# Optimization experiments

Measured on AMD Instinct MI355X. Metric: run time of the kernel, lower is better.

Reference implementation:

```python
import jax, jax.numpy as jnp
import numpy as np

N = 200000   # nodes
E = 800000   # edges
G = 10000    # graphs in batch
H = 128      # hidden_channels
IN_NODE = 26  # 10-2 + 16 + 2
IN_EDGE = 13  # 4-3 + 8 + 2*2


def setup_inputs() -> dict:
    key = jax.random.key(0)
    ks = jax.random.split(key, 30)
    f = lambda i, shape: (jax.random.normal(ks[i], shape, jnp.float32) * 0.1)
    inp = {}
    inp['atom_num'] = jax.random.randint(ks[0], (N,), 0, 119)
    inp['atom_arom'] = jax.random.randint(ks[1], (N,), 0, 2)
    inp['x_cont'] = f(2, (N, 8))
    inp['bond_type'] = jax.random.randint(ks[3], (E,), 0, 22)
    inp['edge_cont'] = f(4, (E, 1))
    inp['bond_conj'] = jax.random.randint(ks[5], (E,), 0, 2)
    inp['bond_arom'] = jax.random.randint(ks[6], (E,), 0, 2)
    inp['edge_index'] = jax.random.randint(ks[7], (2, E), 0, N)
    inp['batch'] = jnp.sort(jax.random.randint(ks[8], (N,), 0, G))
    # embeddings (padding rows zeroed, matching padding_idx)
    inp['atom_emb'] = f(9, (119, 16)).at[0].set(0.0)
    inp['bond_emb'] = f(10, (22, 8)).at[0].set(0.0)
    inp['bool_emb'] = f(11, (3, 2)).at[2].set(0.0)
    # GATv2 layer 1 (gnn1)
    inp['Wl1'] = f(12, (IN_NODE, H)); inp['bl1'] = f(13, (H,))
    inp['Wr1'] = f(14, (IN_NODE, H)); inp['br1'] = f(15, (H,))
    inp['We1'] = f(16, (IN_EDGE, H))
    inp['att1'] = f(17, (H,)); inp['bias1'] = f(18, (H,))
    # GATv2 shared layer (gnn) -- used for layers 2 and 3 with the SAME weights
    inp['Wl2'] = f(19, (H, H)); inp['bl2'] = f(20, (H,))
    inp['Wr2'] = f(21, (H, H)); inp['br2'] = f(22, (H,))
    inp['We2'] = f(23, (IN_EDGE, H))
    inp['att2'] = f(24, (H,)); inp['bias2'] = f(25, (H,))
    return inp


def _gatv2(x, src, dst, ea, Wl, bl, Wr, br, We, att, bias):
    """PyG GATv2Conv, heads=1, add_self_loops=True, fill_value='mean'."""
    n = x.shape[0]
    # self-loop edge features = mean of incoming edge features per node
    deg = jax.ops.segment_sum(jnp.ones((src.shape[0],), x.dtype), dst, num_segments=n)
    ea_mean = jax.ops.segment_sum(ea, dst, num_segments=n) / jnp.clip(deg, 1.0)[:, None]
    loop = jnp.arange(n, dtype=src.dtype)
    s = jnp.concatenate([src, loop])
    d = jnp.concatenate([dst, loop])
    ea_full = jnp.concatenate([ea, ea_mean], axis=0)
    xl = x @ Wl + bl   # source transform
    xr = x @ Wr + br   # destination transform
    m = xl[s] + xr[d] + ea_full @ We           # [E+N, H]
    m = jax.nn.leaky_relu(m, 0.2)
    logits = m @ att                            # [E+N]
    mx = jax.ops.segment_max(logits, d, num_segments=n)
    a = jnp.exp(logits - mx[d])
    denom = jax.ops.segment_sum(a, d, num_segments=n)
    alpha = a / denom[d]
    out = jax.ops.segment_sum(alpha[:, None] * xl[s], d, num_segments=n)
    return out + bias


def reference(atom_num, atom_arom, x_cont, bond_type, edge_cont, bond_conj,
              bond_arom, edge_index, batch, atom_emb, bond_emb, bool_emb,
              Wl1, bl1, Wr1, br1, We1, att1, bias1,
              Wl2, bl2, Wr2, br2, We2, att2, bias2):
    src, dst = edge_index[0], edge_index[1]
    x = jnp.concatenate([atom_emb[atom_num], x_cont, bool_emb[atom_arom]], axis=1)  # [N,26]
    ea = jnp.concatenate([bond_emb[bond_type], edge_cont,
                          bool_emb[bond_conj], bool_emb[bond_arom]], axis=1)        # [E,13]
    h = jax.nn.relu(_gatv2(x, src, dst, ea, Wl1, bl1, Wr1, br1, We1, att1, bias1))
    # num_layers_gnn=3 -> shared-weight layer applied twice (dropout off in eval)
    h = jax.nn.relu(_gatv2(h, src, dst, ea, Wl2, bl2, Wr2, br2, We2, att2, bias2))
    h = jax.nn.relu(_gatv2(h, src, dst, ea, Wl2, bl2, Wr2, br2, We2, att2, bias2))
    pooled = jax.ops.segment_max(h, batch, num_segments=G)  # global_max_pool
    pooled = jnp.where(jnp.isfinite(pooled), pooled, 0.0)   # guard empty graphs
    return pooled
```

## Files before the change

kernel.cpp:

```cpp
#include <hip/hip_runtime.h>
#include <hip/hip_bf16.h>
#include <cstdint>
#include <cstdio>


typedef __attribute__((ext_vector_type(8))) short bf16x8;
typedef __attribute__((ext_vector_type(8))) unsigned short u16x8;
typedef __attribute__((ext_vector_type(4))) float f32x4;

#define TBT_S 132

static __device__ __forceinline__ float leaky02(float v) { return v > 0.f ? v : 0.2f * v; }
static __device__ __forceinline__ float b2f(unsigned short u) {
    return __uint_as_float(((unsigned)u) << 16);
}
static __device__ __forceinline__ unsigned short f2b(float f) {
    __hip_bfloat16 h = __float2bfloat16(f);
    return *(unsigned short*)&h;
}


__global__ __launch_bounds__(256) void prep_init(
    int* __restrict__ degcnt, int n_degcnt,
    int* __restrict__ outz, int n_out,
    const float* __restrict__ Wl2, const float* __restrict__ Wr2,
    __hip_bfloat16* __restrict__ Wp,
    const float* __restrict__ Wl1, const float* __restrict__ Wr1,
    __hip_bfloat16* __restrict__ Wp1,
    const int* __restrict__ atom_num, const int* __restrict__ atom_arom,
    const float* __restrict__ x_cont, const float* __restrict__ atom_emb,
    const float* __restrict__ bool_emb, __hip_bfloat16* __restrict__ Xf, int N,
    int e_z1, int e_z2, int e_pw, int e_pw1)
{
    int b = blockIdx.x;
    if (b < e_z1) {
        int i = b * 256 + threadIdx.x;
        if (i < n_degcnt) degcnt[i] = 0;
    } else if (b < e_z2) {
        int i = (b - e_z1) * 256 + threadIdx.x;
        if (i < n_out) outz[i] = 0;
    } else if (b < e_pw) {
        int idx = (b - e_z2) * 256 + threadIdx.x;
        int j    = idx & 7;
        int lane = (idx >> 3) & 63;
        int ks   = (idx >> 9) & 3;
        int nt   = idx >> 11;
        int k = ks * 32 + ((lane >> 4) << 3) + j;
        int n = nt * 16 + (lane & 15);
        float v = (n < 128) ? Wl2[k * 128 + n] : Wr2[k * 128 + (n - 128)];
        Wp[idx] = __float2bfloat16(v);
    } else if (b < e_pw1) {
        int idx = (b - e_pw) * 256 + threadIdx.x;
        int j    = idx & 7;
        int lane = (idx >> 3) & 63;
        int ntc  = idx >> 9;
        int k = ((lane >> 4) << 3) + j;
        int n = ntc * 16 + (lane & 15);
        float v = 0.f;
        if (k < 26) v = (n < 128) ? Wl1[k * 128 + n] : Wr1[k * 128 + (n - 128)];
        Wp1[idx] = __float2bfloat16(v);
    } else {
        int n = (b - e_pw1) * 256 + threadIdx.x;
        if (n >= N) return;
        int an = atom_num[n], am = atom_arom[n];
        unsigned short v[32];
#pragma unroll
        for (int k = 0; k < 16; k++) v[k] = f2b(atom_emb[an * 16 + k]);
#pragma unroll
        for (int k = 0; k < 8; k++)  v[16 + k] = f2b(x_cont[(size_t)n * 8 + k]);
        v[24] = f2b(bool_emb[am * 2]);
        v[25] = f2b(bool_emb[am * 2 + 1]);
#pragma unroll
        for (int k = 26; k < 32; k++) v[k] = 0;
        unsigned short* dst = (unsigned short*)Xf + (size_t)n * 32;
#pragma unroll
        for (int q = 0; q < 4; q++)
            *(u16x8*)(dst + q * 8) = *(const u16x8*)&v[q * 8];
    }
}


__global__ __launch_bounds__(256) void count_deg(
    const int* __restrict__ dst, int* __restrict__ deg, int E)
{
    int e = blockIdx.x * 256 + threadIdx.x;
    if (e < E) atomicAdd(&deg[dst[e]], 1);
}

#define SORT_BLK 1024

__global__ __launch_bounds__(256) void sort_hist(
    const int* __restrict__ deg, int* __restrict__ block_hist, int N)
{
    __shared__ int h[512];
    for (int i = threadIdx.x; i < 512; i += 256) h[i] = 0;
    __syncthreads();
    int base = blockIdx.x * SORT_BLK;
#pragma unroll
    for (int k = 0; k < 4; k++) {
        int n = base + k * 256 + threadIdx.x;
        if (n < N) {
            int d = deg[n]; if (d > 511) d = 511;
            atomicAdd(&h[d], 1);
        }
    }
    __syncthreads();
    for (int i = threadIdx.x; i < 512; i += 256)
        block_hist[blockIdx.x * 512 + i] = h[i];
}

__global__ __launch_bounds__(512) void sort_scan(
    int* __restrict__ block_hist, int* __restrict__ bin_base,
    int* __restrict__ edge_base, int nsb)
{
    __shared__ int s[512];
    int t = threadIdx.x;
    int acc = 0;
    for (int b = 0; b < nsb; b++) {
        int v = block_hist[b * 512 + t];
        block_hist[b * 512 + t] = acc;
        acc += v;
    }
    s[t] = acc;
    __syncthreads();
    for (int off = 1; off < 512; off <<= 1) {
        int x = (t >= off) ? s[t - off] : 0;
        __syncthreads();
        s[t] += x;
        __syncthreads();
    }
    bin_base[t] = s[t] - acc;
    __syncthreads();
    int ec = acc * t;
    s[t] = ec;
    __syncthreads();
    for (int off = 1; off < 512; off <<= 1) {
        int x = (t >= off) ? s[t - off] : 0;
        __syncthreads();
        s[t] += x;
        __syncthreads();
    }
    edge_base[t] = s[t] - ec;
}

__global__ __launch_bounds__(256) void sort_scatter(
    const int* __restrict__ deg, const int* __restrict__ block_hist,
    const int* __restrict__ bin_base, const int* __restrict__ edge_base,
    int4* __restrict__ meta, int* __restrict__ nrp, int N)
{
    __shared__ int h[512];
    for (int i = threadIdx.x; i < 512; i += 256) h[i] = 0;
    __syncthreads();
    int bs = blockIdx.x;
    int base = bs * SORT_BLK;
#pragma unroll
    for (int k = 0; k < 4; k++) {
        int n = base + k * 256 + threadIdx.x;
        if (n < N) {
            int d = deg[n]; if (d > 511) d = 511;
            int r = atomicAdd(&h[d], 1);
            int posInBin = block_hist[bs * 512 + d] + r;
            int pos = bin_base[d] + posInBin;
            int rp = edge_base[d] + posInBin * d;
            int4 m; m.x = rp; m.y = d; m.z = n; m.w = 0;
            meta[pos] = m;
            nrp[n] = rp;
        }
    }
}

__global__ __launch_bounds__(256) void csr_fill(
    const int* __restrict__ src, const int* __restrict__ dst,
    const int* __restrict__ bond_type, const float* __restrict__ edge_cont,
    const int* __restrict__ bond_conj, const int* __restrict__ bond_arom,
    const int* __restrict__ nrp, int* __restrict__ cnt,
    int4* __restrict__ csr_rec, int E)
{
    int e = blockIdx.x * 256 + threadIdx.x;
    if (e >= E) return;
    int d = dst[e];
    int pos = nrp[d] + atomicAdd(&cnt[d], 1);
    int codes = (bond_type[e] & 0xFF) | ((bond_conj[e] & 1) << 8) | ((bond_arom[e] & 1) << 16);
    int4 rec;
    rec.x = src[e];
    rec.y = codes;
    rec.z = __float_as_int(edge_cont[e]);
    rec.w = 0;
    csr_rec[pos] = rec;
}


__global__ __launch_bounds__(256) void gemm_mfma1(
    const __hip_bfloat16* __restrict__ Xf,
    const __hip_bfloat16* __restrict__ Wp,
    const float* __restrict__ bl, const float* __restrict__ br,
    __hip_bfloat16* __restrict__ XL, __hip_bfloat16* __restrict__ XR, int N)
{
    __shared__ unsigned short sT[64 * 256];
    int lane = threadIdx.x & 63;
    int wave = threadIdx.x >> 6;
    int row0 = blockIdx.x * 64;
    int m_lane = lane & 15;
    int quad = lane >> 4;
    const unsigned short* Xu = (const unsigned short*)Xf;
    const unsigned short* Wu = (const unsigned short*)Wp;

    f32x4 acc[4][4];
#pragma unroll
    for (int mt = 0; mt < 4; mt++)
#pragma unroll
        for (int nt = 0; nt < 4; nt++) acc[mt][nt] = (f32x4){0.f, 0.f, 0.f, 0.f};

    bf16x8 a[4], b[4];
#pragma unroll
    for (int mt = 0; mt < 4; mt++)
        a[mt] = *(const bf16x8*)(Xu + (size_t)(row0 + mt * 16 + m_lane) * 32 + quad * 8);
#pragma unroll
    for (int nt = 0; nt < 4; nt++)
        b[nt] = *(const bf16x8*)(Wu + ((wave * 4 + nt) * 64 + lane) * 8);
#pragma unroll
    for (int mt = 0; mt < 4; mt++)
#pragma unroll
        for (int nt = 0; nt < 4; nt++)
            acc[mt][nt] = __builtin_amdgcn_mfma_f32_16x16x32_bf16(
                a[mt], b[nt], acc[mt][nt], 0, 0, 0);

#pragma unroll
    for (int nt = 0; nt < 4; nt++) {
        int col = wave * 64 + nt * 16 + m_lane;
        float bv = (col < 128) ? bl[col] : br[col - 128];
#pragma unroll
        for (int mt = 0; mt < 4; mt++) {
            int rbase = mt * 16 + quad * 4;
#pragma unroll
            for (int reg = 0; reg < 4; reg++)
                sT[(rbase + reg) * 256 + col] = f2b(acc[mt][nt][reg] + bv);
        }
    }

    __syncthreads();

    unsigned short* XLu = (unsigned short*)XL;
    unsigned short* XRu = (unsigned short*)XR;
    int t = threadIdx.x;
#pragma unroll
    for (int q = 0; q < 4; q++) {
        int s = t * 32 + q * 8;
        int r = s >> 7, c = s & 127;
        *(u16x8*)(XLu + (size_t)(row0 + r) * 128 + c) = *(const u16x8*)&sT[r * 256 + c];
        *(u16x8*)(XRu + (size_t)(row0 + r) * 128 + c) = *(const u16x8*)&sT[r * 256 + 128 + c];
    }
}

__global__ __launch_bounds__(256) void gemm_mfma(
    const __hip_bfloat16* H,
    const __hip_bfloat16* __restrict__ Wp,
    const float* __restrict__ bl, const float* __restrict__ br,
    __hip_bfloat16* __restrict__ XL, __hip_bfloat16* XR, int N)
{
    __shared__ unsigned short sT[64 * 256];
    int lane = threadIdx.x & 63;
    int wave = threadIdx.x >> 6;
    int row0 = blockIdx.x * 64;
    int m_lane = lane & 15;
    int quad = lane >> 4;
    const unsigned short* Hu = (const unsigned short*)H;
    const unsigned short* Wu = (const unsigned short*)Wp;

    f32x4 acc[4][4];
#pragma unroll
    for (int mt = 0; mt < 4; mt++)
#pragma unroll
        for (int nt = 0; nt < 4; nt++) acc[mt][nt] = (f32x4){0.f, 0.f, 0.f, 0.f};

#pragma unroll
    for (int ks = 0; ks < 4; ks++) {
        int koff = ks * 32 + quad * 8;
        bf16x8 a[4], b[4];
#pragma unroll
        for (int mt = 0; mt < 4; mt++)
            a[mt] = *(const bf16x8*)(Hu + (size_t)(row0 + mt * 16 + m_lane) * 128 + koff);
#pragma unroll
        for (int nt = 0; nt < 4; nt++)
            b[nt] = *(const bf16x8*)(Wu + ((((wave * 4 + nt) * 4) + ks) * 64 + lane) * 8);
#pragma unroll
        for (int mt = 0; mt < 4; mt++)
#pragma unroll
            for (int nt = 0; nt < 4; nt++)
                acc[mt][nt] = __builtin_amdgcn_mfma_f32_16x16x32_bf16(
                    a[mt], b[nt], acc[mt][nt], 0, 0, 0);
    }

#pragma unroll
    for (int nt = 0; nt < 4; nt++) {
        int col = wave * 64 + nt * 16 + m_lane;
        float bv = (col < 128) ? bl[col] : br[col - 128];
#pragma unroll
        for (int mt = 0; mt < 4; mt++) {
            int rbase = mt * 16 + quad * 4;
#pragma unroll
            for (int reg = 0; reg < 4; reg++)
                sT[(rbase + reg) * 256 + col] = f2b(acc[mt][nt][reg] + bv);
        }
    }

    __syncthreads();

    unsigned short* XLu = (unsigned short*)XL;
    unsigned short* XRu = (unsigned short*)XR;
    int t = threadIdx.x;
#pragma unroll
    for (int q = 0; q < 4; q++) {
        int s = t * 32 + q * 8;
        int r = s >> 7, c = s & 127;
        *(u16x8*)(XLu + (size_t)(row0 + r) * 128 + c) = *(const u16x8*)&sT[r * 256 + c];
        *(u16x8*)(XRu + (size_t)(row0 + r) * 128 + c) = *(const u16x8*)&sT[r * 256 + 128 + c];
    }
}

__global__ __launch_bounds__(256) void gat_fused(
    const int4* __restrict__ meta, const int4* __restrict__ csr_rec,
    const float* __restrict__ bond_emb, const float* __restrict__ bool_emb,
    const __hip_bfloat16* __restrict__ XL, const __hip_bfloat16* XR,
    const float* __restrict__ We,
    const float* __restrict__ att,
    const float* __restrict__ bias,
    __hip_bfloat16* OUT, int N)
{
    __shared__ float sTbt[22 * TBT_S];
    __shared__ float sTca[4 * TBT_S];
    __shared__ float sW8[128];

    for (int i = threadIdx.x; i < 22 * 128; i += 256) {
        int bt = i >> 7, c = i & 127;
        float s = 0.f;
#pragma unroll
        for (int k = 0; k < 8; k++) s = fmaf(bond_emb[bt * 8 + k], We[k * 128 + c], s);
        sTbt[bt * TBT_S + c] = s;
    }
    for (int i = threadIdx.x; i < 4 * 128; i += 256) {
        int idx = i >> 7, c = i & 127;
        int cj = idx >> 1, ar = idx & 1;
        float s = bool_emb[cj * 2]     * We[9 * 128 + c]
                + bool_emb[cj * 2 + 1] * We[10 * 128 + c]
                + bool_emb[ar * 2]     * We[11 * 128 + c]
                + bool_emb[ar * 2 + 1] * We[12 * 128 + c];
        sTca[idx * TBT_S + c] = s;
    }
    if (threadIdx.x < 128) sW8[threadIdx.x] = We[8 * 128 + threadIdx.x];
    __syncthreads();

    int lane = threadIdx.x & 63;
    int wave = threadIdx.x >> 6;
    int sl   = lane & 15;
    int sw   = lane >> 4;
    int cbase = sl * 8;

    float a8[8], bs8[8], w88[8];
    {
        float4 t0 = *(const float4*)&att[cbase],  t1 = *(const float4*)&att[cbase + 4];
        float4 u0 = *(const float4*)&bias[cbase], u1 = *(const float4*)&bias[cbase + 4];
        float4 v0 = *(const float4*)&sW8[cbase],  v1 = *(const float4*)&sW8[cbase + 4];
#pragma unroll
        for (int i = 0; i < 4; i++) {
            a8[i] = (&t0.x)[i];  a8[i + 4] = (&t1.x)[i];
            bs8[i] = (&u0.x)[i]; bs8[i + 4] = (&u1.x)[i];
            w88[i] = (&v0.x)[i]; w88[i + 4] = (&v1.x)[i];
        }
    }

    const unsigned short* XLu = (const unsigned short*)XL;
    const unsigned short* XRu = (const unsigned short*)XR;
    unsigned short* OUTu = (unsigned short*)OUT;

    int group = (blockIdx.x * 4 + wave) * 4 + sw;
    int stride = gridDim.x * 16;

    int4 mt;
    if (group < N) mt = meta[group];

    for (int idx = group; idx < N; idx += stride) {
        int rp = mt.x, dg = mt.y, n = mt.z;
        u16x8 uxr = *(const u16x8*)(XRu + (size_t)n * 128 + cbase);
        u16x8 un  = *(const u16x8*)(XLu + (size_t)n * 128 + cbase);
        int nidx = idx + stride;
        int4 mt_n = meta[(nidx < N) ? nidx : idx];

        float xr[8];
#pragma unroll
        for (int i = 0; i < 8; i++) xr[i] = b2f(uxr[i]);

        float runs = 0.f;
        float acc[8], ets[8];
#pragma unroll
        for (int i = 0; i < 8; i++) { acc[i] = 0.f; ets[i] = 0.f; }

        for (int j = 0; j < dg; j += 4) {
            int cnt = dg - j; if (cnt > 4) cnt = 4;
            int4 rec[4];
#pragma unroll
            for (int jj = 0; jj < 4; jj++)
                if (jj < cnt) rec[jj] = csr_rec[rp + j + jj];
            u16x8 uv[4];
#pragma unroll
            for (int jj = 0; jj < 4; jj++)
                if (jj < cnt)
                    uv[jj] = *(const u16x8*)(XLu + (size_t)rec[jj].x * 128 + cbase);

            float part[4];
#pragma unroll
            for (int jj = 0; jj < 4; jj++) {
                if (jj >= cnt) continue;
                int bt = rec[jj].y & 0xFF;
                int ca = (((rec[jj].y >> 8) & 1) << 1) | ((rec[jj].y >> 16) & 1);
                float ec = __int_as_float(rec[jj].z);
                const float* tb = &sTbt[bt * TBT_S + cbase];
                const float* tc = &sTca[ca * TBT_S + cbase];
                float p = 0.f;
#pragma unroll
                for (int i = 0; i < 8; i++) {
                    float et = fmaf(ec, w88[i], tb[i] + tc[i]);
                    ets[i] += et;
                    float m = leaky02(xr[i] + b2f(uv[jj][i]) + et);
                    p = fmaf(m, a8[i], p);
                }
                p += __shfl_xor(p, 1);
                p += __shfl_xor(p, 2);
                p += __shfl_xor(p, 4);
                p += __shfl_xor(p, 8);
                part[jj] = p;
            }
#pragma unroll
            for (int jj = 0; jj < 4; jj++) {
                if (jj >= cnt) continue;
                float wgt = __expf(part[jj]);
                runs += wgt;
#pragma unroll
                for (int i = 0; i < 8; i++)
                    acc[i] = fmaf(wgt, b2f(uv[jj][i]), acc[i]);
            }
        }

        {
            float invd = 1.f / (float)(dg > 0 ? dg : 1);
            float p = 0.f;
#pragma unroll
            for (int i = 0; i < 8; i++) {
                float m = leaky02(xr[i] + b2f(un[i]) + ets[i] * invd);
                p = fmaf(m, a8[i], p);
            }
            p += __shfl_xor(p, 1);
            p += __shfl_xor(p, 2);
            p += __shfl_xor(p, 4);
            p += __shfl_xor(p, 8);
            float wgt = __expf(p);
            runs += wgt;
#pragma unroll
            for (int i = 0; i < 8; i++)
                acc[i] = fmaf(wgt, b2f(un[i]), acc[i]);
        }

        float inv = 1.f / runs;
        u16x8 o;
#pragma unroll
        for (int i = 0; i < 8; i++)
            o[i] = f2b(fmaxf(fmaf(acc[i], inv, bs8[i]), 0.f));
        *(u16x8*)(OUTu + (size_t)n * 128 + cbase) = o;

        mt = mt_n;
    }
}

__global__ __launch_bounds__(128) void pool_max(
    const __hip_bfloat16* __restrict__ H, const int* __restrict__ batch,
    float* __restrict__ out, int N)
{
    int c = threadIdx.x;
    int n0 = blockIdx.x * 64;
    int nend = n0 + 64; if (nend > N) nend = N;
    const unsigned short* Hu = (const unsigned short*)H;
    int g_cur = -1;
    float acc = 0.f;
    for (int n = n0; n < nend; ++n) {
        int g = batch[n];
        if (g != g_cur) {
            if (g_cur >= 0)
                atomicMax((int*)out + (size_t)g_cur * 128 + c, __float_as_int(acc));
            g_cur = g;
            acc = 0.f;
        }
        acc = fmaxf(acc, b2f(Hu[(size_t)n * 128 + c]));
    }
    if (g_cur >= 0)
        atomicMax((int*)out + (size_t)g_cur * 128 + c, __float_as_int(acc));
}


static inline size_t align_up(size_t x, size_t a) { return (x + a - 1) & ~(a - 1); }
static inline int cdiv(int a, int b) { return (a + b - 1) / b; }

extern "C" void kernel_launch(void* const* d_in, const int* in_sizes, int n_in,
                              void* d_out, int out_size, void* d_ws, size_t ws_size,
                              hipStream_t stream)
{
    const int N = in_sizes[0];
    const int E = in_sizes[3];

    const int*   atom_num  = (const int*)d_in[0];
    const int*   atom_arom = (const int*)d_in[1];
    const float* x_cont    = (const float*)d_in[2];
    const int*   bond_type = (const int*)d_in[3];
    const float* edge_cont = (const float*)d_in[4];
    const int*   bond_conj = (const int*)d_in[5];
    const int*   bond_arom = (const int*)d_in[6];
    const int*   e_src     = (const int*)d_in[7];
    const int*   e_dst     = e_src + E;
    const int*   batch     = (const int*)d_in[8];
    const float* atom_emb  = (const float*)d_in[9];
    const float* bond_emb  = (const float*)d_in[10];
    const float* bool_emb  = (const float*)d_in[11];
    const float* Wl1 = (const float*)d_in[12]; const float* bl1 = (const float*)d_in[13];
    const float* Wr1 = (const float*)d_in[14]; const float* br1 = (const float*)d_in[15];
    const float* We1 = (const float*)d_in[16]; const float* att1 = (const float*)d_in[17];
    const float* bias1 = (const float*)d_in[18];
    const float* Wl2 = (const float*)d_in[19]; const float* bl2 = (const float*)d_in[20];
    const float* Wr2 = (const float*)d_in[21]; const float* br2 = (const float*)d_in[22];
    const float* We2 = (const float*)d_in[23]; const float* att2 = (const float*)d_in[24];
    const float* bias2 = (const float*)d_in[25];
    float* out = (float*)d_out;

    const int nsb = cdiv(N, SORT_BLK);

    char* w = (char*)d_ws;
    size_t off = 0;
    auto alloc = [&](size_t bytes) {
        void* p = w + off;
        off = align_up(off + bytes, 256);
        return p;
    };
    __hip_bfloat16* A  = (__hip_bfloat16*)alloc((size_t)N * 128 * 2);
    __hip_bfloat16* B  = (__hip_bfloat16*)alloc((size_t)N * 128 * 2);
    __hip_bfloat16* Xf = (__hip_bfloat16*)alloc((size_t)N * 32 * 2);
    __hip_bfloat16* Wp = (__hip_bfloat16*)alloc((size_t)32768 * 2);
    __hip_bfloat16* Wp1= (__hip_bfloat16*)alloc((size_t)8192 * 2);
    int*   degcnt  = (int*)alloc((size_t)2 * N * 4);
    int*   deg     = degcnt;
    int*   cnt     = degcnt + N;
    int4*  csr_rec = (int4*)alloc((size_t)E * 16);
    int4*  meta    = (int4*)alloc((size_t)N * 16);
    int*   nrp     = (int*)alloc((size_t)N * 4);
    int*   block_hist = (int*)alloc((size_t)nsb * 512 * 4);
    int*   bin_base   = (int*)alloc(512 * 4);
    int*   edge_base  = (int*)alloc(512 * 4);
    size_t required = off;

    fprintf(stderr, "[GNN] ws_size=%zu required=%zu%s\n", ws_size, required,
            ws_size < required ? "  INSUFFICIENT - skipping" : "");
    if (ws_size < required) return;

    int bz1 = cdiv(2 * N, 256);
    int bz2 = cdiv(out_size, 256);
    int bpw = 32768 / 256;
    int bpw1 = 8192 / 256;
    int bbx = cdiv(N, 256);
    int e_z1 = bz1, e_z2 = e_z1 + bz2, e_pw = e_z2 + bpw, e_pw1 = e_pw + bpw1;
    prep_init<<<e_pw1 + bbx, 256, 0, stream>>>(
        degcnt, 2 * N, (int*)out, out_size,
        Wl2, Wr2, Wp, Wl1, Wr1, Wp1,
        atom_num, atom_arom, x_cont, atom_emb, bool_emb, Xf, N,
        e_z1, e_z2, e_pw, e_pw1);

    count_deg<<<cdiv(E, 256), 256, 0, stream>>>(e_dst, deg, E);
    sort_hist<<<nsb, 256, 0, stream>>>(deg, block_hist, N);
    sort_scan<<<1, 512, 0, stream>>>(block_hist, bin_base, edge_base, nsb);
    sort_scatter<<<nsb, 256, 0, stream>>>(deg, block_hist, bin_base, edge_base,
                                          meta, nrp, N);
    csr_fill<<<cdiv(E, 256), 256, 0, stream>>>(e_src, e_dst, bond_type, edge_cont,
                                               bond_conj, bond_arom, nrp, cnt,
                                               csr_rec, E);

    const int fused_blocks = 1536;

    gemm_mfma1<<<N / 64, 256, 0, stream>>>(Xf, Wp1, bl1, br1, A, B, N);
    gat_fused<<<fused_blocks, 256, 0, stream>>>(
        meta, csr_rec, bond_emb, bool_emb, A, B, We1, att1, bias1, B, N);

    for (int layer = 0; layer < 2; ++layer) {
        gemm_mfma<<<N / 64, 256, 0, stream>>>(B, Wp, bl2, br2, A, B, N);
        gat_fused<<<fused_blocks, 256, 0, stream>>>(
            meta, csr_rec, bond_emb, bool_emb, A, B, We2, att2, bias2, B, N);
    }

    pool_max<<<cdiv(N, 64), 128, 0, stream>>>(B, batch, out, N);
}
```

Baseline: 710.3 us.

## Software-pipeline CSR record and XR prefetch in GAT gather, set occupancy hint

Restructures the gat_fused edge loop so the next chunk of CSR records (including the first chunk of the next node) and the next node's XR row are loaded one iteration ahead, with meta prefetched two nodes ahead. The aim is to hide the dependent-load latency of record then XL-row fetches. It also adds a min-blocks launch bound of 4 and unrolls the sort_scan histogram loop by four. The pipelining raises register pressure, which the launch bound may force into spills, and it issues a few redundant clamped loads at chunk boundaries.

```diff
diff --git a/kernel.cpp b/kernel.cpp
--- a/kernel.cpp
+++ b/kernel.cpp
@@ -116,7 +116,18 @@
     __shared__ int s[512];
     int t = threadIdx.x;
     int acc = 0;
-    for (int b = 0; b < nsb; b++) {
+    int b = 0;
+    for (; b + 4 <= nsb; b += 4) {
+        int v0 = block_hist[(b + 0) * 512 + t];
+        int v1 = block_hist[(b + 1) * 512 + t];
+        int v2 = block_hist[(b + 2) * 512 + t];
+        int v3 = block_hist[(b + 3) * 512 + t];
+        block_hist[(b + 0) * 512 + t] = acc; acc += v0;
+        block_hist[(b + 1) * 512 + t] = acc; acc += v1;
+        block_hist[(b + 2) * 512 + t] = acc; acc += v2;
+        block_hist[(b + 3) * 512 + t] = acc; acc += v3;
+    }
+    for (; b < nsb; b++) {
         int v = block_hist[b * 512 + t];
         block_hist[b * 512 + t] = acc;
         acc += v;
@@ -318,7 +329,7 @@
     }
 }
 
-__global__ __launch_bounds__(256) void gat_fused(
+__global__ __launch_bounds__(256, 4) void gat_fused(
     const int4* __restrict__ meta, const int4* __restrict__ csr_rec,
     const float* __restrict__ bond_emb, const float* __restrict__ bool_emb,
     const __hip_bfloat16* __restrict__ XL, const __hip_bfloat16* XR,
@@ -376,15 +387,27 @@
     int group = (blockIdx.x * 4 + wave) * 4 + sw;
     int stride = gridDim.x * 16;
 
-    int4 mt;
-    if (group < N) mt = meta[group];
+    if (group >= N) return;
+
+    int4 mt  = meta[group];
+    int ni   = group + stride;
+    int4 mtn = meta[(ni < N) ? ni : (N - 1)];
+    int4 rc[4];
+    {
+        int rp0 = mt.x, dg0 = mt.y;
+#pragma unroll
+        for (int jj = 0; jj < 4; jj++)
+            rc[jj] = csr_rec[rp0 + (jj < dg0 ? jj : 0)];
+    }
+    u16x8 uxr = *(const u16x8*)(XRu + (size_t)mt.z * 128 + cbase);
 
     for (int idx = group; idx < N; idx += stride) {
-        int rp = mt.x, dg = mt.y, n = mt.z;
-        u16x8 uxr = *(const u16x8*)(XRu + (size_t)n * 128 + cbase);
-        u16x8 un  = *(const u16x8*)(XLu + (size_t)n * 128 + cbase);
-        int nidx = idx + stride;
-        int4 mt_n = meta[(nidx < N) ? nidx : idx];
+        const int rp = mt.x, dg = mt.y, n = mt.z;
+
+        u16x8 un = *(const u16x8*)(XLu + (size_t)n * 128 + cbase);
+        int i2 = idx + 2 * stride;
+        int4 mt2 = meta[(i2 < N) ? i2 : (N - 1)];
+        u16x8 uxr_n = *(const u16x8*)(XRu + (size_t)mtn.z * 128 + cbase);
 
         float xr[8];
 #pragma unroll
@@ -395,25 +418,32 @@
 #pragma unroll
         for (int i = 0; i < 8; i++) { acc[i] = 0.f; ets[i] = 0.f; }
 
-        for (int j = 0; j < dg; j += 4) {
-            int cnt = dg - j; if (cnt > 4) cnt = 4;
-            int4 rec[4];
-#pragma unroll
-            for (int jj = 0; jj < 4; jj++)
-                if (jj < cnt) rec[jj] = csr_rec[rp + j + jj];
+        int j = 0;
+        do {
+            int cnt = dg - j;
+            cnt = cnt < 0 ? 0 : (cnt > 4 ? 4 : cnt);
+
             u16x8 uv[4];
 #pragma unroll
             for (int jj = 0; jj < 4; jj++)
                 if (jj < cnt)
-                    uv[jj] = *(const u16x8*)(XLu + (size_t)rec[jj].x * 128 + cbase);
+                    uv[jj] = *(const u16x8*)(XLu + (size_t)rc[jj].x * 128 + cbase);
+
+            int innode = (j + 4 < dg);
+            int nb = innode ? (rp + j + 4) : mtn.x;
+            int nd = innode ? (dg - j - 4) : mtn.y;
+            int4 rn[4];
+#pragma unroll
+            for (int jj = 0; jj < 4; jj++)
+                rn[jj] = csr_rec[nb + (jj < nd ? jj : 0)];
 
             float part[4];
 #pragma unroll
             for (int jj = 0; jj < 4; jj++) {
                 if (jj >= cnt) continue;
-                int bt = rec[jj].y & 0xFF;
-                int ca = (((rec[jj].y >> 8) & 1) << 1) | ((rec[jj].y >> 16) & 1);
-                float ec = __int_as_float(rec[jj].z);
+                int bt = rc[jj].y & 0xFF;
+                int ca = (((rc[jj].y >> 8) & 1) << 1) | ((rc[jj].y >> 16) & 1);
+                float ec = __int_as_float(rc[jj].z);
                 const float* tb = &sTbt[bt * TBT_S + cbase];
                 const float* tc = &sTca[ca * TBT_S + cbase];
                 float p = 0.f;
@@ -439,7 +469,10 @@
                 for (int i = 0; i < 8; i++)
                     acc[i] = fmaf(wgt, b2f(uv[jj][i]), acc[i]);
             }
-        }
+#pragma unroll
+            for (int jj = 0; jj < 4; jj++) rc[jj] = rn[jj];
+            j += 4;
+        } while (j < dg);
 
         {
             float invd = 1.f / (float)(dg > 0 ? dg : 1);
@@ -467,7 +500,7 @@
             o[i] = f2b(fmaxf(fmaf(acc[i], inv, bs8[i]), 0.f));
         *(u16x8*)(OUTu + (size_t)n * 128 + cbase) = o;
 
-        mt = mt_n;
+        mt = mtn; mtn = mt2; uxr = uxr_n;
     }
 }
 
```

Result: slower. 1.177 ms (+65.7%).
